# Kernel optimization log

Hardware: AMD Instinct MI355X
Metric: run time of the kernel (lower is better)

## Reference

```python
import jax, jax.numpy as jnp
import numpy as np

TEMPORAL_WIDTH = 4  # hardcoded in GRUBlock


def causal_conv1d(x, w, b):
    """Depthwise causal temporal conv. x:[B,T,R], w:[4,R], b:[R].
    out[t] = sum_i w[i] * x[t - 3 + i] + b (zero left padding)."""
    T = x.shape[1]
    xp = jnp.pad(x, ((0, 0), (TEMPORAL_WIDTH - 1, 0), (0, 0)))
    y = b
    for i in range(TEMPORAL_WIDTH):  # tiny fixed loop over 4 taps
        y = y + w[i] * xp[:, i:i + T]
    return y


def linear_scan(a, b):
    """h_t = a_t * h_{t-1} + b_t with h_{-1}=0, via associative scan over time."""
    def comb(e1, e2):
        a1, b1 = e1
        a2, b2 = e2
        return a2 * a1, a2 * b1 + b2
    _, h = jax.lax.associative_scan(comb, (a, b), axis=1)
    return h


def setup_inputs() -> dict:
    key = jax.random.key(0)
    k1, k2, k3, k4 = jax.random.split(key, 4)
    B, T, H, R = 4, 8192, 1024, 1024
    x = jax.random.normal(k1, (B, T, H), dtype=jnp.float32)
    # lecun init: N(0, 1/sqrt(d_in)); torch Linear weight is [out, in]
    w_zh = jax.random.normal(k2, (2 * R, H), dtype=jnp.float32) / np.sqrt(H)
    w_out = jax.random.normal(k3, (H, R), dtype=jnp.float32) / np.sqrt(R)
    conv_w = jax.random.normal(k4, (TEMPORAL_WIDTH, R), dtype=jnp.float32) / np.sqrt(TEMPORAL_WIDTH)
    conv_b = jnp.zeros((R,), dtype=jnp.float32)
    return {"x": x, "w_zh": w_zh, "w_out": w_out, "conv_w": conv_w, "conv_b": conv_b}


def reference(x, w_zh, w_out, conv_w, conv_b):
    # residual causal conv
    x = x + causal_conv1d(x, conv_w, conv_b)
    # fused z/h projection: [B,T,H] @ [H,2R]
    zh = jnp.einsum('bth,rh->btr', x, w_zh)
    z, h = jnp.split(zh, 2, axis=-1)
    z = jax.nn.sigmoid(z)
    # GRU-style linear recurrence: h_t = (1-z_t) h_{t-1} + z_t h~_t
    h_o = linear_scan(1.0 - z, z * h)
    return jnp.einsum('btr,hr->bth', h_o, w_out)
```

## Files before the change

kernel.cpp:

```cpp
#include <hip/hip_runtime.h>

typedef __bf16 bf16x8 __attribute__((ext_vector_type(8)));
typedef __bf16 bf16x4 __attribute__((ext_vector_type(4)));
typedef float  f32x4  __attribute__((ext_vector_type(4)));
typedef float  f32x16 __attribute__((ext_vector_type(16)));

static constexpr int Bb = 4, T = 8192, H = 1024, R = 1024;
static constexpr int BT = Bb * T;
static constexpr int N1 = 2 * R;
static constexpr int CH = 64;
static constexpr int L  = T / CH;

__device__ __forceinline__ void g2lds16(const void* g, void* l) {
  __builtin_amdgcn_global_load_lds(
      (const __attribute__((address_space(1))) unsigned int*)g,
      (__attribute__((address_space(3))) unsigned int*)l, 16, 0, 0);
}

__global__ __launch_bounds__(256) void cast_f32_bf16(const float* __restrict__ in,
                                                     __bf16* __restrict__ out, int n4) {
  int i = blockIdx.x * 256 + threadIdx.x;
  if (i >= n4) return;
  const f32x4 v = *(const f32x4*)(in + (size_t)i * 4);
  bf16x4 o;
  o[0] = (__bf16)v[0]; o[1] = (__bf16)v[1]; o[2] = (__bf16)v[2]; o[3] = (__bf16)v[3];
  *(bf16x4*)(out + (size_t)i * 4) = o;
}

__global__ __launch_bounds__(256) void conv_residual_cast(const float* __restrict__ x,
                                                          const float* __restrict__ cw,
                                                          const float* __restrict__ cb,
                                                          __bf16* __restrict__ xc) {
  const size_t i4 = (size_t)blockIdx.x * 256 + threadIdx.x;
  const size_t v  = i4 * 4;
  const int    h  = (int)(v & (size_t)(H - 1));
  const size_t bt = v >> 10;
  const int    t  = (int)(bt & (size_t)(T - 1));
  f32x4 acc = *(const f32x4*)(cb + h);
  const f32x4 xv = *(const f32x4*)(x + v);
#pragma unroll
  for (int i = 0; i < 4; ++i) {
    const int tt = t - 3 + i;
    if (tt >= 0) {
      const f32x4 xi = *(const f32x4*)(x + (bt - 3 + i) * H + h);
      const f32x4 wi = *(const f32x4*)(cw + i * H + h);
      acc += wi * xi;
    }
  }
  acc += xv;
  bf16x4 o;
  o[0] = (__bf16)acc[0]; o[1] = (__bf16)acc[1]; o[2] = (__bf16)acc[2]; o[3] = (__bf16)acc[3];
  *(bf16x4*)(xc + v) = o;
}

template <typename OUT_T>
__global__ __launch_bounds__(256) void gemm_bt(const __bf16* __restrict__ A,
                                               const __bf16* __restrict__ Bm,
                                               OUT_T* __restrict__ C,
                                               int M, int N, int K) {
  __shared__ __align__(16) __bf16 sA[128 * 64];
  __shared__ __align__(16) __bf16 sB[128 * 64];
  const int tid  = threadIdx.x;
  const int wave = tid >> 6;
  const int lane = tid & 63;
  const int ln = lane & 31;
  const int kb = lane >> 5;
  const int bm0 = blockIdx.y * 128;
  const int bn0 = blockIdx.x * 128;
  const int wm = (wave >> 1) * 64;
  const int wn = (wave & 1) * 64;

  f32x16 acc[2][2] = {};

  int srow[4], sgc[4], sldsE[4];
#pragma unroll
  for (int c = 0; c < 4; ++c) {
    const int li = c * 256 + tid;
    srow[c] = li >> 3;
    sgc[c]  = (li & 7) ^ (srow[c] & 7);
    sldsE[c] = (c * 256 + (tid & ~63)) * 8;
  }

  for (int k0 = 0; k0 < K; k0 += 64) {
#pragma unroll
    for (int c = 0; c < 4; ++c) {
      g2lds16(A  + (size_t)(bm0 + srow[c]) * K + k0 + sgc[c] * 8, sA + sldsE[c]);
      g2lds16(Bm + (size_t)(bn0 + srow[c]) * K + k0 + sgc[c] * 8, sB + sldsE[c]);
    }
    __syncthreads();
#pragma unroll
    for (int ks = 0; ks < 4; ++ks) {
      bf16x8 af[2], bfr[2];
#pragma unroll
      for (int i = 0; i < 2; ++i) {
        const int ra = wm + i * 32 + ln;
        af[i]  = *(const bf16x8*)(sA + ra * 64 + (((2 * ks + kb) ^ (ra & 7)) * 8));
        const int rb = wn + i * 32 + ln;
        bfr[i] = *(const bf16x8*)(sB + rb * 64 + (((2 * ks + kb) ^ (rb & 7)) * 8));
      }
#pragma unroll
      for (int i = 0; i < 2; ++i)
#pragma unroll
        for (int j = 0; j < 2; ++j)
          acc[i][j] = __builtin_amdgcn_mfma_f32_32x32x16_bf16(af[i], bfr[j], acc[i][j], 0, 0, 0);
    }
    __syncthreads();
  }
#pragma unroll
  for (int i = 0; i < 2; ++i)
#pragma unroll
    for (int j = 0; j < 2; ++j) {
      const int col = bn0 + wn + j * 32 + ln;
#pragma unroll
      for (int rr = 0; rr < 16; ++rr) {
        const int row = bm0 + wm + i * 32 + (rr & 3) + 8 * (rr >> 2) + 4 * kb;
        C[(size_t)row * N + col] = (OUT_T)acc[i][j][rr];
      }
    }
}

__global__ __launch_bounds__(256) void scan_pass1(const __bf16* __restrict__ zh,
                                                  float* __restrict__ aggA,
                                                  float* __restrict__ aggB) {
  const int r = blockIdx.x * 256 + threadIdx.x;
  const int c = blockIdx.y;
  const int b = blockIdx.z;
  size_t base = ((size_t)b * T + (size_t)c * L) * N1 + r;
  float Aacc = 1.f, Bacc = 0.f;
#pragma unroll 4
  for (int t = 0; t < L; ++t) {
    const float s  = (float)zh[base];
    const float hh = (float)zh[base + R];
    base += N1;
    const float z = 1.f / (1.f + __expf(-s));
    const float a = 1.f - z;
    Bacc = a * Bacc + z * hh;
    Aacc *= a;
  }
  const size_t o = ((size_t)b * CH + c) * R + r;
  aggA[o] = Aacc;
  aggB[o] = Bacc;
}

__global__ __launch_bounds__(256) void scan_pass2(const float* __restrict__ aggA,
                                                  const float* __restrict__ aggB,
                                                  float* __restrict__ carry) {
  const int idx = blockIdx.x * 256 + threadIdx.x;
  const int b = idx >> 10;
  const int r = idx & (R - 1);
  float h = 0.f;
#pragma unroll 8
  for (int c = 0; c < CH; ++c) {
    const size_t o = ((size_t)b * CH + c) * R + r;
    carry[o] = h;
    h = aggA[o] * h + aggB[o];
  }
}

__global__ __launch_bounds__(256) void scan_pass3(const __bf16* __restrict__ zh,
                                                  const float* __restrict__ carry,
                                                  __bf16* __restrict__ ho) {
  const int r = blockIdx.x * 256 + threadIdx.x;
  const int c = blockIdx.y;
  const int b = blockIdx.z;
  size_t base  = ((size_t)b * T + (size_t)c * L) * N1 + r;
  size_t obase = ((size_t)b * T + (size_t)c * L) * R + r;
  float h = carry[((size_t)b * CH + c) * R + r];
#pragma unroll 4
  for (int t = 0; t < L; ++t) {
    const float s  = (float)zh[base];
    const float hh = (float)zh[base + R];
    base += N1;
    const float z = 1.f / (1.f + __expf(-s));
    h = (1.f - z) * h + z * hh;
    ho[obase] = (__bf16)h;
    obase += R;
  }
}

extern "C" void kernel_launch(void* const* d_in, const int* in_sizes, int n_in,
                              void* d_out, int out_size, void* d_ws, size_t ws_size,
                              hipStream_t stream) {
  const float* x      = (const float*)d_in[0];
  const float* w_zh   = (const float*)d_in[1];
  const float* w_out  = (const float*)d_in[2];
  const float* conv_w = (const float*)d_in[3];
  const float* conv_b = (const float*)d_in[4];
  float* out = (float*)d_out;

  char* ws = (char*)d_ws;
  size_t off = 0;
  __bf16* wzh_b  = (__bf16*)(ws + off); off += (size_t)N1 * H * 2;
  __bf16* wout_b = (__bf16*)(ws + off); off += (size_t)H * R * 2;
  __bf16* xc     = (__bf16*)(ws + off); off += (size_t)BT * H * 2;
  __bf16* zh     = (__bf16*)(ws + off); off += (size_t)BT * N1 * 2;
  float*  aggA   = (float*)(ws + off);  off += (size_t)Bb * CH * R * 4;
  float*  aggB   = (float*)(ws + off);  off += (size_t)Bb * CH * R * 4;
  float*  carry  = (float*)(ws + off);  off += (size_t)Bb * CH * R * 4;
  __bf16* ho = xc;

  cast_f32_bf16<<<(N1 * H / 4 + 255) / 256, 256, 0, stream>>>(w_zh, wzh_b, N1 * H / 4);
  cast_f32_bf16<<<(H * R / 4 + 255) / 256, 256, 0, stream>>>(w_out, wout_b, H * R / 4);
  conv_residual_cast<<<BT * H / 4 / 256, 256, 0, stream>>>(x, conv_w, conv_b, xc);
  gemm_bt<__bf16><<<dim3(N1 / 128, BT / 128), 256, 0, stream>>>(xc, wzh_b, zh, BT, N1, H);
  scan_pass1<<<dim3(R / 256, CH, Bb), 256, 0, stream>>>(zh, aggA, aggB);
  scan_pass2<<<Bb * R / 256, 256, 0, stream>>>(aggA, aggB, carry);
  scan_pass3<<<dim3(R / 256, CH, Bb), 256, 0, stream>>>(zh, carry, ho);
  gemm_bt<float><<<dim3(H / 128, BT / 128), 256, 0, stream>>>(ho, wout_b, out, BT, H, R);
}
```

Baseline: 611.5 us.

## Replace GEMM with 256x256 double-buffered, phase-pipelined MFMA kernel

Swaps the 128x128 single-buffered GEMM for a 256x256 tile kernel with 8 waves. It double-buffers LDS, interleaves the next tiles' global-to-LDS loads with four MFMA phases, raises wave priority during MFMA, and remaps workgroup IDs for cache locality. The aim is to hide memory latency and raise data reuse in both projections. In exchange it needs 128KB of LDS per block, more registers, and hand-placed waitcnt/barrier logic that could be fragile.

```diff
diff --git a/kernel.cpp b/kernel.cpp
--- a/kernel.cpp
+++ b/kernel.cpp
@@ -3,7 +3,6 @@
 typedef __bf16 bf16x8 __attribute__((ext_vector_type(8)));
 typedef __bf16 bf16x4 __attribute__((ext_vector_type(4)));
 typedef float  f32x4  __attribute__((ext_vector_type(4)));
-typedef float  f32x16 __attribute__((ext_vector_type(16)));
 
 static constexpr int Bb = 4, T = 8192, H = 1024, R = 1024;
 static constexpr int BT = Bb * T;
@@ -53,69 +52,112 @@
   *(bf16x4*)(xc + v) = o;
 }
 
+
+#define STG_A(buf, k0, ro) g2lds16(aBase + (size_t)(r + (ro)) * K + (k0), \
+                                   &sA[buf][(w8 + (ro)) * 64])
+#define STG_B(buf, k0, ro) g2lds16(bBase + (size_t)(rB + (ro)) * K + (k0), \
+                                   &sB[buf][(w8B + (ro)) * 64])
+#define STAGE_A02(buf, kt) do { const int k0_ = (kt) * 64; STG_A(buf, k0_, 0);  STG_A(buf, k0_, 128); } while (0)
+#define STAGE_A13(buf, kt) do { const int k0_ = (kt) * 64; STG_A(buf, k0_, 64); STG_A(buf, k0_, 192); } while (0)
+#define STAGE_BEV(buf, kt) do { const int k0_ = (kt) * 64; STG_B(buf, k0_, 0);  STG_B(buf, k0_, 128); } while (0)
+#define STAGE_BOD(buf, kt) do { const int k0_ = (kt) * 64; STG_B(buf, k0_, 32); STG_B(buf, k0_, 160); } while (0)
+
+#define PHASE(MQ, NQ, STAGE_STMT, W4) do {                                           \
+    bf16x8 af_[4][2], bf_[2][2];                                                     \
+    _Pragma("unroll") for (int i_ = 0; i_ < 4; ++i_) {                               \
+      const int rt_ = aRowBase + (MQ) * 64 + i_ * 16;                                \
+      _Pragma("unroll") for (int ks_ = 0; ks_ < 2; ++ks_)                            \
+        af_[i_][ks_] = *(const bf16x8*)&sAc[rt_ * 64 + (((ks_ * 4 + kg) ^ (rt_ & 7)) * 8)]; \
+    }                                                                                \
+    _Pragma("unroll") for (int j_ = 0; j_ < 2; ++j_) {                               \
+      const int rt_ = bRowBase + (NQ) * 32 + j_ * 16;                                \
+      _Pragma("unroll") for (int ks_ = 0; ks_ < 2; ++ks_)                            \
+        bf_[j_][ks_] = *(const bf16x8*)&sBc[rt_ * 64 + (((ks_ * 4 + kg) ^ (rt_ & 7)) * 8)]; \
+    }                                                                                \
+    STAGE_STMT;                                                                      \
+    asm volatile("s_barrier" ::: "memory");                                          \
+    asm volatile("s_waitcnt lgkmcnt(0)" ::: "memory");                               \
+    __builtin_amdgcn_s_setprio(1);                                                   \
+    _Pragma("unroll") for (int i_ = 0; i_ < 4; ++i_)                                 \
+      _Pragma("unroll") for (int j_ = 0; j_ < 2; ++j_)                               \
+        _Pragma("unroll") for (int ks_ = 0; ks_ < 2; ++ks_)                          \
+          acc[(MQ) * 4 + i_][(NQ) * 2 + j_] = __builtin_amdgcn_mfma_f32_16x16x32_bf16( \
+              af_[i_][ks_], bf_[j_][ks_], acc[(MQ) * 4 + i_][(NQ) * 2 + j_], 0, 0, 0); \
+    __builtin_amdgcn_s_setprio(0);                                                   \
+    if (W4) asm volatile("s_waitcnt vmcnt(4)" ::: "memory");                         \
+    asm volatile("s_barrier" ::: "memory");                                          \
+  } while (0)
+
 template <typename OUT_T>
-__global__ __launch_bounds__(256) void gemm_bt(const __bf16* __restrict__ A,
-                                               const __bf16* __restrict__ Bm,
-                                               OUT_T* __restrict__ C,
-                                               int M, int N, int K) {
-  __shared__ __align__(16) __bf16 sA[128 * 64];
-  __shared__ __align__(16) __bf16 sB[128 * 64];
+__global__ __launch_bounds__(512, 2) void gemm256(const __bf16* __restrict__ A,
+                                                  const __bf16* __restrict__ Bm,
+                                                  OUT_T* __restrict__ C,
+                                                  int M, int N, int K, int nbx) {
+  __shared__ __align__(16) __bf16 sA[2][256 * 64];
+  __shared__ __align__(16) __bf16 sB[2][256 * 64];
   const int tid  = threadIdx.x;
   const int wave = tid >> 6;
   const int lane = tid & 63;
-  const int ln = lane & 31;
-  const int kb = lane >> 5;
-  const int bm0 = blockIdx.y * 128;
-  const int bn0 = blockIdx.x * 128;
-  const int wm = (wave >> 1) * 64;
-  const int wn = (wave & 1) * 64;
-
-  f32x16 acc[2][2] = {};
-
-  int srow[4], sgc[4], sldsE[4];
-#pragma unroll
-  for (int c = 0; c < 4; ++c) {
-    const int li = c * 256 + tid;
-    srow[c] = li >> 3;
-    sgc[c]  = (li & 7) ^ (srow[c] & 7);
-    sldsE[c] = (c * 256 + (tid & ~63)) * 8;
-  }
-
-  for (int k0 = 0; k0 < K; k0 += 64) {
-#pragma unroll
-    for (int c = 0; c < 4; ++c) {
-      g2lds16(A  + (size_t)(bm0 + srow[c]) * K + k0 + sgc[c] * 8, sA + sldsE[c]);
-      g2lds16(Bm + (size_t)(bn0 + srow[c]) * K + k0 + sgc[c] * 8, sB + sldsE[c]);
-    }
-    __syncthreads();
-#pragma unroll
-    for (int ks = 0; ks < 4; ++ks) {
-      bf16x8 af[2], bfr[2];
-#pragma unroll
-      for (int i = 0; i < 2; ++i) {
-        const int ra = wm + i * 32 + ln;
-        af[i]  = *(const bf16x8*)(sA + ra * 64 + (((2 * ks + kb) ^ (ra & 7)) * 8));
-        const int rb = wn + i * 32 + ln;
-        bfr[i] = *(const bf16x8*)(sB + rb * 64 + (((2 * ks + kb) ^ (rb & 7)) * 8));
-      }
-#pragma unroll
-      for (int i = 0; i < 2; ++i)
-#pragma unroll
-        for (int j = 0; j < 2; ++j)
-          acc[i][j] = __builtin_amdgcn_mfma_f32_32x32x16_bf16(af[i], bfr[j], acc[i][j], 0, 0, 0);
-    }
-    __syncthreads();
-  }
-#pragma unroll
-  for (int i = 0; i < 2; ++i)
-#pragma unroll
-    for (int j = 0; j < 2; ++j) {
-      const int col = bn0 + wn + j * 32 + ln;
-#pragma unroll
-      for (int rr = 0; rr < 16; ++rr) {
-        const int row = bm0 + wm + i * 32 + (rr & 3) + 8 * (rr >> 2) + 4 * kb;
-        C[(size_t)row * N + col] = (OUT_T)acc[i][j][rr];
-      }
+  const int wm = wave >> 2;
+  const int wn = wave & 3;
+
+  const int nwg = gridDim.x;
+  int wg = blockIdx.x;
+  wg = (wg & 7) * (nwg >> 3) + (wg >> 3);
+  const int bm0 = (wg / nbx) * 256;
+  const int bn0 = (wg % nbx) * 256;
+
+  const int NT = K >> 6;
+
+  const int r   = tid >> 3;
+  const int sgc = (tid & 7) ^ (r & 7);
+  const int rB  = r + (r & 32);
+  const int w8  = wave * 8;
+  const int w8B = w8 + (w8 & 32);
+  const __bf16* aBase = A  + (size_t)bm0 * K + sgc * 8;
+  const __bf16* bBase = Bm + (size_t)bn0 * K + sgc * 8;
+
+  const int l15 = lane & 15;
+  const int kg  = lane >> 4;
+  const int aRowBase = wm * 128 + l15;
+  const int bRowBase = wn * 64 + l15;
+
+  f32x4 acc[8][4] = {};
+
+  STAGE_BEV(0, 0);
+  STAGE_A02(0, 0);
+  STAGE_A13(0, 0);
+  STAGE_BOD(0, 0);
+  {
+    const int k1 = NT > 1 ? 1 : 0;
+    STAGE_BEV(1, k1);
+    STAGE_A02(1, k1);
+  }
+  asm volatile("s_waitcnt vmcnt(4)" ::: "memory");
+  asm volatile("s_barrier" ::: "memory");
+
+  for (int kt = 0; kt < NT; ++kt) {
+    const int cur = kt & 1, nxt = cur ^ 1;
+    const int kt1 = (kt + 1 < NT) ? kt + 1 : NT - 1;
+    const int kt2 = (kt + 2 < NT) ? kt + 2 : NT - 1;
+    const __bf16* sAc = sA[cur];
+    const __bf16* sBc = sB[cur];
+    PHASE(0, 0, STAGE_A13(nxt, kt1), 0);
+    PHASE(1, 0, STAGE_BOD(nxt, kt1), 0);
+    PHASE(0, 1, STAGE_BEV(cur, kt2), 0);
+    PHASE(1, 1, STAGE_A02(cur, kt2), 1);
+  }
+
+  const int orow0 = bm0 + wm * 128 + kg * 4;
+  const int ocol0 = bn0 + wn * 64 + l15;
+#pragma unroll
+  for (int mi = 0; mi < 8; ++mi)
+#pragma unroll
+    for (int nj = 0; nj < 4; ++nj) {
+      const size_t rbase = (size_t)(orow0 + mi * 16);
+#pragma unroll
+      for (int rr = 0; rr < 4; ++rr)
+        C[(rbase + rr) * N + (ocol0 + nj * 16)] = (OUT_T)acc[mi][nj][rr];
     }
 }
 
@@ -202,9 +244,9 @@
   cast_f32_bf16<<<(N1 * H / 4 + 255) / 256, 256, 0, stream>>>(w_zh, wzh_b, N1 * H / 4);
   cast_f32_bf16<<<(H * R / 4 + 255) / 256, 256, 0, stream>>>(w_out, wout_b, H * R / 4);
   conv_residual_cast<<<BT * H / 4 / 256, 256, 0, stream>>>(x, conv_w, conv_b, xc);
-  gemm_bt<__bf16><<<dim3(N1 / 128, BT / 128), 256, 0, stream>>>(xc, wzh_b, zh, BT, N1, H);
+  gemm256<__bf16><<<(BT / 256) * (N1 / 256), 512, 0, stream>>>(xc, wzh_b, zh, BT, N1, H, N1 / 256);
   scan_pass1<<<dim3(R / 256, CH, Bb), 256, 0, stream>>>(zh, aggA, aggB);
   scan_pass2<<<Bb * R / 256, 256, 0, stream>>>(aggA, aggB, carry);
   scan_pass3<<<dim3(R / 256, CH, Bb), 256, 0, stream>>>(zh, carry, ho);
-  gemm_bt<float><<<dim3(H / 128, BT / 128), 256, 0, stream>>>(ho, wout_b, out, BT, H, R);
-}
+  gemm256<float><<<(BT / 256) * (H / 256), 512, 0, stream>>>(ho, wout_b, out, BT, H, R, H / 256);
+}
```

Result: faster. 587.2 us (-4.0%).
